# Performance work log

Measured on AMD Instinct MI355X. Metric: run time of the kernel, lower is better.

Reference implementation:

```python
import jax, jax.numpy as jnp
import numpy as np

EPS = 1e-5
QB = 128.0  # 2**(bit-1), bit=8

def _int8_wrap(q):
    # Emulate torch's .to(torch.int8) two's-complement wrap (e.g. 128 -> -128).
    return jnp.mod(q + 128.0, 256.0) - 128.0

def setup_inputs() -> dict:
    key = jax.random.key(0)
    k1, k2, k3 = jax.random.split(key, 3)
    x = jax.random.normal(k1, (4, 2048, 2048), dtype=jnp.float32)
    weights = jax.random.normal(k2, (8192, 2048), dtype=jnp.float32)
    bias = jax.random.normal(k3, (8192,), dtype=jnp.float32)
    return {"x": x, "weights": weights, "bias": bias}

def reference(x, weights, bias):
    in_features = x.shape[-1]
    out_features = weights.shape[0]
    # LayerNorm over last dim, no affine (F.layer_norm defaults, eps=1e-5)
    mu = jnp.mean(x, axis=-1, keepdims=True)
    var = jnp.mean(jnp.square(x - mu), axis=-1, keepdims=True)
    input_norm = (x - mu) * jax.lax.rsqrt(var + EPS)
    # absmax int8 activation quant (nl_next=False path)
    max_val = jnp.max(jnp.abs(input_norm))
    q = _int8_wrap(jnp.round(input_norm * (QB / max_val)))
    dequant = max_val / QB
    # weight sign-binarization around the mean
    weight_quant = jnp.sign(weights - jnp.mean(weights))
    # quantized matmul + dequant scales + bias
    out = jnp.einsum('bsd,od->bso', q, weight_quant)  # [B,S,out]
    beta = jnp.sum(jnp.abs(weights)) / (in_features * out_features)
    out = out * (dequant * beta) + bias
    return out
```

## Files before the change

kernel.cpp:

```cpp
#include <hip/hip_runtime.h>


using i32x4 = __attribute__((ext_vector_type(4))) int;
using i32x16 = __attribute__((ext_vector_type(16))) int;

typedef const __attribute__((address_space(1))) void cg_void;
typedef __attribute__((address_space(3))) void lds_void;

#define K_DIM 2048
#define N_DIM 8192
#define M_DIM 8192
#define NELEM_W 16777216


__global__ __launch_bounds__(256) void pass1(const float* __restrict__ x,
                                             const float4* __restrict__ w4,
                                             float* __restrict__ mu_arr,
                                             float* __restrict__ rstd_arr,
                                             float* __restrict__ rowmax,
                                             double2* __restrict__ part) {
    __shared__ double sbd[8];
    __shared__ float sb1[4];
    __shared__ float sb2[8];
    const int bid = blockIdx.x, t = threadIdx.x;
    const int lane = t & 63, wv = t >> 6;
    if (bid < 1024) {
        double s = 0.0, a = 0.0;
        for (int i = bid * 256 + t; i < NELEM_W / 4; i += 1024 * 256) {
            float4 v = w4[i];
            s += (double)v.x + (double)v.y + (double)v.z + (double)v.w;
            a += fabs((double)v.x) + fabs((double)v.y) + fabs((double)v.z) + fabs((double)v.w);
        }
        for (int o = 32; o; o >>= 1) { s += __shfl_xor(s, o); a += __shfl_xor(a, o); }
        if (lane == 0) { sbd[wv] = s; sbd[4 + wv] = a; }
        __syncthreads();
        if (t == 0) {
            double2 r;
            r.x = sbd[0] + sbd[1] + sbd[2] + sbd[3];
            r.y = sbd[4] + sbd[5] + sbd[6] + sbd[7];
            part[bid] = r;
        }
    } else {
        const int row = bid - 1024;
        const float4* xr = (const float4*)x + (size_t)row * 512;
        float4 v0 = xr[t], v1 = xr[t + 256];
        float s = v0.x + v0.y + v0.z + v0.w + v1.x + v1.y + v1.z + v1.w;
        for (int o = 32; o; o >>= 1) s += __shfl_xor(s, o);
        if (lane == 0) sb1[wv] = s;
        __syncthreads();
        float mu = (sb1[0] + sb1[1] + sb1[2] + sb1[3]) * (1.0f / 2048.0f);
        float ssq = 0.f, md = 0.f, d;
        d = v0.x - mu; ssq += d * d; md = fmaxf(md, fabsf(d));
        d = v0.y - mu; ssq += d * d; md = fmaxf(md, fabsf(d));
        d = v0.z - mu; ssq += d * d; md = fmaxf(md, fabsf(d));
        d = v0.w - mu; ssq += d * d; md = fmaxf(md, fabsf(d));
        d = v1.x - mu; ssq += d * d; md = fmaxf(md, fabsf(d));
        d = v1.y - mu; ssq += d * d; md = fmaxf(md, fabsf(d));
        d = v1.z - mu; ssq += d * d; md = fmaxf(md, fabsf(d));
        d = v1.w - mu; ssq += d * d; md = fmaxf(md, fabsf(d));
        for (int o = 32; o; o >>= 1) {
            ssq += __shfl_xor(ssq, o);
            md = fmaxf(md, __shfl_xor(md, o));
        }
        if (lane == 0) { sb2[wv] = ssq; sb2[4 + wv] = md; }
        __syncthreads();
        if (t == 0) {
            float var = (sb2[0] + sb2[1] + sb2[2] + sb2[3]) * (1.0f / 2048.0f);
            float rstd = 1.0f / sqrtf(var + 1e-5f);
            mu_arr[row] = mu;
            rstd_arr[row] = rstd;
            rowmax[row] = fmaxf(fmaxf(sb2[4], sb2[5]), fmaxf(sb2[6], sb2[7])) * rstd;
        }
    }
}

__global__ __launch_bounds__(256) void wred2(const double2* __restrict__ part,
                                             const float* __restrict__ rowmax,
                                             unsigned* __restrict__ scal) {
    double s = 0.0, a = 0.0;
    float m = 0.f;
    const int t = threadIdx.x, lane = t & 63, wv = t >> 6;
    for (int i = t; i < 1024; i += 256) { double2 p = part[i]; s += p.x; a += p.y; }
    for (int i = t; i < 8192; i += 256) m = fmaxf(m, rowmax[i]);
    for (int o = 32; o; o >>= 1) {
        s += __shfl_xor(s, o); a += __shfl_xor(a, o);
        m = fmaxf(m, __shfl_xor(m, o));
    }
    __shared__ double sbd[8];
    __shared__ float sbm[4];
    if (lane == 0) { sbd[wv] = s; sbd[4 + wv] = a; sbm[wv] = m; }
    __syncthreads();
    if (t == 0) {
        double st = sbd[0] + sbd[1] + sbd[2] + sbd[3];
        double at = sbd[4] + sbd[5] + sbd[6] + sbd[7];
        ((float*)scal)[0] = fmaxf(fmaxf(sbm[0], sbm[1]), fmaxf(sbm[2], sbm[3]));
        ((float*)scal)[1] = (float)(st / (double)NELEM_W);
        ((float*)scal)[2] = (float)(at / (double)NELEM_W);
    }
}

__device__ __forceinline__ int sgn8(float d) { return (d > 0.f) ? 1 : ((d < 0.f) ? -1 : 0); }

__global__ __launch_bounds__(256) void pass2(const float* __restrict__ x,
                                             const float4* __restrict__ w4,
                                             const float* __restrict__ mu_arr,
                                             const float* __restrict__ rstd_arr,
                                             const unsigned* __restrict__ scal,
                                             signed char* __restrict__ q,
                                             int4* __restrict__ wq4) {
    const int bid = blockIdx.x, t = threadIdx.x;
    if (bid < 1024) {
        float wm = ((const float*)scal)[1];
        for (int i = bid * 256 + t; i < NELEM_W / 16; i += 1024 * 256) {
            int words[4];
            #pragma unroll
            for (int jj = 0; jj < 4; ++jj) {
                float4 v = w4[i * 4 + jj];
                int b0 = sgn8(v.x - wm) & 255, b1 = sgn8(v.y - wm) & 255;
                int b2 = sgn8(v.z - wm) & 255, b3 = sgn8(v.w - wm) & 255;
                words[jj] = b0 | (b1 << 8) | (b2 << 16) | (b3 << 24);
            }
            wq4[i] = make_int4(words[0], words[1], words[2], words[3]);
        }
    } else {
        const int row = bid - 1024;
        float mu = mu_arr[row], rstd = rstd_arr[row];
        float s = 128.0f / ((const float*)scal)[0];
        const float4* xr = (const float4*)x + (size_t)row * 512;
        float4 v0 = xr[2 * t], v1 = xr[2 * t + 1];
        float xs[8] = {v0.x, v0.y, v0.z, v0.w, v1.x, v1.y, v1.z, v1.w};
        int b[8];
        #pragma unroll
        for (int j = 0; j < 8; ++j) {
            float norm = (xs[j] - mu) * rstd;
            int qi = (int)rintf(norm * s);
            b[j] = qi & 255;
        }
        int w0 = b[0] | (b[1] << 8) | (b[2] << 16) | (b[3] << 24);
        int w1 = b[4] | (b[5] << 8) | (b[6] << 16) | (b[7] << 24);
        ((int2*)(q + (size_t)row * 2048))[t] = make_int2(w0, w1);
    }
}

#define LD16(p) (*(const i32x4*)(p))
#define TILE_BYTES 24576

#define STAGE(koff, sbase)                                                                  \
    do {                                                                                    \
        __builtin_amdgcn_global_load_lds((cg_void*)(gA + (koff)),                           \
            (lds_void*)(lds + (sbase) + w * 2048), 16, 0, 0);                               \
        __builtin_amdgcn_global_load_lds((cg_void*)(gA + 8 * K_DIM + (koff)),               \
            (lds_void*)(lds + (sbase) + w * 2048 + 1024), 16, 0, 0);                        \
        __builtin_amdgcn_global_load_lds((cg_void*)(gB + (koff)),                           \
            (lds_void*)(lds + (sbase) + 16384 + w * 1024), 16, 0, 0);                       \
    } while (0)

__global__ __launch_bounds__(512, 4) void gemm_i8(const signed char* __restrict__ A,
                                                  const signed char* __restrict__ B,
                                                  const float* __restrict__ bias,
                                                  const unsigned* __restrict__ scal,
                                                  float* __restrict__ C) {
    __shared__ alignas(16) char lds[49152];
    const int t = threadIdx.x, w = t >> 6, lane = t & 63;

    const int wg = blockIdx.x;
    const int xcd = wg & 7, idx = wg >> 3;
    const int bm = (xcd * 4 + (idx >> 6)) * 256;
    const int bn = (idx & 63) * 128;

    const int wr = w >> 1, wc = w & 1;
    const int r32 = lane & 31, hi = lane >> 5;

    const int uu = (lane & 7) ^ (lane >> 3);
    const int aRow = w * 16 + (lane >> 3) + ((uu >> 2) << 7);
    const int bRow = w * 8 + (lane >> 3) + ((uu >> 2) << 6);
    const int gcol = (uu & 3) << 4;
    const signed char* gA = A + (size_t)(bm + aRow) * K_DIM + gcol;
    const signed char* gB = B + (size_t)(bn + bRow) * K_DIM + gcol;

    const char* aBase = lds + ((wr & 1) * 64 + r32) * 128;
    const char* bBase = lds + 16384 + r32 * 128;
    const int axr = r32 & 7;
    const int aS0 = ((((wr >> 1) << 2) + hi) ^ axr) << 4;
    const int aS1 = ((((wr >> 1) << 2) + 2 + hi) ^ axr) << 4;
    const int bS0 = (((wc << 2) + hi) ^ axr) << 4;
    const int bS1 = (((wc << 2) + 2 + hi) ^ axr) << 4;

    const float scale = (((const float*)scal)[0] * (1.0f / 128.0f)) * ((const float*)scal)[2];

    i32x16 acc[2][2] = {};
    i32x4 a0[2], a1[2], b0[2], b1[2];

    STAGE(0, 0);

    #pragma unroll 2
    for (int kt = 0; kt < 32; ++kt) {
        const int c = (kt & 1) * TILE_BYTES;
        if (kt < 31) {
            STAGE((kt + 1) * 64, ((kt + 1) & 1) * TILE_BYTES);
            asm volatile("s_waitcnt vmcnt(3)" ::: "memory");
        } else {
            asm volatile("s_waitcnt vmcnt(0)" ::: "memory");
        }
        __builtin_amdgcn_s_barrier();

        #pragma unroll
        for (int mb = 0; mb < 2; ++mb) a0[mb] = LD16(aBase + c + mb * 4096 + aS0);
        #pragma unroll
        for (int nb = 0; nb < 2; ++nb) b0[nb] = LD16(bBase + c + nb * 4096 + bS0);
        #pragma unroll
        for (int mb = 0; mb < 2; ++mb) a1[mb] = LD16(aBase + c + mb * 4096 + aS1);
        #pragma unroll
        for (int nb = 0; nb < 2; ++nb) b1[nb] = LD16(bBase + c + nb * 4096 + bS1);
        __builtin_amdgcn_s_setprio(1);
        #pragma unroll
        for (int mb = 0; mb < 2; ++mb)
            #pragma unroll
            for (int nb = 0; nb < 2; ++nb)
                acc[mb][nb] = __builtin_amdgcn_mfma_i32_32x32x32_i8(a0[mb], b0[nb],
                                                                    acc[mb][nb], 0, 0, 0);
        #pragma unroll
        for (int mb = 0; mb < 2; ++mb)
            #pragma unroll
            for (int nb = 0; nb < 2; ++nb)
                acc[mb][nb] = __builtin_amdgcn_mfma_i32_32x32x32_i8(a1[mb], b1[nb],
                                                                    acc[mb][nb], 0, 0, 0);
        __builtin_amdgcn_s_setprio(0);
        __builtin_amdgcn_s_barrier();
    }

    const int colbase = bn + wc * 64;
    float bi[2];
    #pragma unroll
    for (int nb = 0; nb < 2; ++nb) bi[nb] = bias[colbase + nb * 32 + r32];
    #pragma unroll
    for (int mb = 0; mb < 2; ++mb) {
        #pragma unroll
        for (int nb = 0; nb < 2; ++nb) {
            #pragma unroll
            for (int r = 0; r < 16; ++r) {
                int row = bm + wr * 64 + mb * 32 + (r & 3) + 8 * (r >> 2) + 4 * hi;
                int col = colbase + nb * 32 + r32;
                C[(size_t)row * N_DIM + col] = (float)acc[mb][nb][r] * scale + bi[nb];
            }
        }
    }
}

extern "C" void kernel_launch(void* const* d_in, const int* in_sizes, int n_in,
                              void* d_out, int out_size, void* d_ws, size_t ws_size,
                              hipStream_t stream) {
    const float* x = (const float*)d_in[0];
    const float* wts = (const float*)d_in[1];
    const float* bias = (const float*)d_in[2];
    float* out = (float*)d_out;

    char* ws = (char*)d_ws;
    unsigned* scal = (unsigned*)ws;
    double2* part = (double2*)(ws + 1024);
    float* mu = (float*)(ws + 32768);
    float* rstd = (float*)(ws + 65536);
    float* rowmax = (float*)(ws + 98304);
    signed char* q = (signed char*)(ws + 131072);
    signed char* wq = (signed char*)(ws + 131072 + 16777216);

    hipLaunchKernelGGL(pass1, dim3(9216), dim3(256), 0, stream,
                       x, (const float4*)wts, mu, rstd, rowmax, part);
    hipLaunchKernelGGL(wred2, dim3(1), dim3(256), 0, stream, part, rowmax, scal);
    hipLaunchKernelGGL(pass2, dim3(9216), dim3(256), 0, stream,
                       x, (const float4*)wts, mu, rstd, scal, q, (int4*)wq);
    hipLaunchKernelGGL(gemm_i8, dim3(2048), dim3(512), 0, stream,
                       q, wq, bias, scal, out);
}
```

Measured before the change: 226.9 us.

## Load B fragments directly from global into registers, stage only A in LDS

The GEMM no longer stages the binarized weight tile B through shared memory. Each wave loads its B fragments straight from global memory into registers every k-step, while A stays double-buffered in LDS under a new XOR swizzle. The LDS footprint drops from 48KB to 32KB and B's LDS write/read traffic is removed. In exchange, duplicate B global loads across waves (wr rows) rely on L1/L2 hits, and the load latency is exposed inside the loop with only loose vmcnt waits.

```diff
diff --git a/kernel.cpp b/kernel.cpp
--- a/kernel.cpp
+++ b/kernel.cpp
@@ -143,7 +143,7 @@
 }
 
 #define LD16(p) (*(const i32x4*)(p))
-#define TILE_BYTES 24576
+#define TILE_BYTES 16384
 
 #define STAGE(koff, sbase)                                                                  \
     do {                                                                                    \
@@ -151,8 +151,6 @@
             (lds_void*)(lds + (sbase) + w * 2048), 16, 0, 0);                               \
         __builtin_amdgcn_global_load_lds((cg_void*)(gA + 8 * K_DIM + (koff)),               \
             (lds_void*)(lds + (sbase) + w * 2048 + 1024), 16, 0, 0);                        \
-        __builtin_amdgcn_global_load_lds((cg_void*)(gB + (koff)),                           \
-            (lds_void*)(lds + (sbase) + 16384 + w * 1024), 16, 0, 0);                       \
     } while (0)
 
 __global__ __launch_bounds__(512, 4) void gemm_i8(const signed char* __restrict__ A,
@@ -160,7 +158,7 @@
                                                   const float* __restrict__ bias,
                                                   const unsigned* __restrict__ scal,
                                                   float* __restrict__ C) {
-    __shared__ alignas(16) char lds[49152];
+    __shared__ alignas(16) char lds[32768];
     const int t = threadIdx.x, w = t >> 6, lane = t & 63;
 
     const int wg = blockIdx.x;
@@ -171,59 +169,70 @@
     const int wr = w >> 1, wc = w & 1;
     const int r32 = lane & 31, hi = lane >> 5;
 
-    const int uu = (lane & 7) ^ (lane >> 3);
-    const int aRow = w * 16 + (lane >> 3) + ((uu >> 2) << 7);
-    const int bRow = w * 8 + (lane >> 3) + ((uu >> 2) << 6);
-    const int gcol = (uu & 3) << 4;
-    const signed char* gA = A + (size_t)(bm + aRow) * K_DIM + gcol;
-    const signed char* gB = B + (size_t)(bn + bRow) * K_DIM + gcol;
+    const int g0 = lane >> 3, s0 = lane & 7;
+    const int u0 = s0 ^ g0 ^ (((w * 2) & 3) << 1);
+    const int u1 = s0 ^ g0 ^ (((w * 2 + 1) & 3) << 1);
+    const int aRow0 = w * 16 + g0 + ((u0 >> 2) << 7);
+    const int aRow1 = w * 16 + 8 + g0 + ((u1 >> 2) << 7);
+    const signed char* gA  = A + (size_t)(bm + aRow0) * K_DIM + ((u0 & 3) << 4);
+    const signed char* gA1 = A + (size_t)(bm + aRow1) * K_DIM + ((u1 & 3) << 4) - 8 * K_DIM;
+    #define gA_J1 gA1
+
+    const signed char* gBf = B + (size_t)(bn + wc * 64 + r32) * K_DIM + hi * 16;
 
     const char* aBase = lds + ((wr & 1) * 64 + r32) * 128;
-    const char* bBase = lds + 16384 + r32 * 128;
-    const int axr = r32 & 7;
-    const int aS0 = ((((wr >> 1) << 2) + hi) ^ axr) << 4;
-    const int aS1 = ((((wr >> 1) << 2) + 2 + hi) ^ axr) << 4;
-    const int bS0 = (((wc << 2) + hi) ^ axr) << 4;
-    const int bS1 = (((wc << 2) + 2 + hi) ^ axr) << 4;
+    const int aperm = (r32 & 7) ^ (((r32 >> 3) & 3) << 1);
+    const int aS0 = ((((wr >> 1) << 2) + hi) ^ aperm) << 4;
+    const int aS1 = ((((wr >> 1) << 2) + 2 + hi) ^ aperm) << 4;
 
     const float scale = (((const float*)scal)[0] * (1.0f / 128.0f)) * ((const float*)scal)[2];
 
     i32x16 acc[2][2] = {};
-    i32x4 a0[2], a1[2], b0[2], b1[2];
-
-    STAGE(0, 0);
+    i32x4 af0[2], af1[2], bc[2][2];
+
+    {
+        __builtin_amdgcn_global_load_lds((cg_void*)(gA), (lds_void*)(lds + w * 2048), 16, 0, 0);
+        __builtin_amdgcn_global_load_lds((cg_void*)(gA1 + 8 * K_DIM),
+                                         (lds_void*)(lds + w * 2048 + 1024), 16, 0, 0);
+    }
 
     #pragma unroll 2
     for (int kt = 0; kt < 32; ++kt) {
         const int c = (kt & 1) * TILE_BYTES;
+        #pragma unroll
+        for (int nb = 0; nb < 2; ++nb)
+            #pragma unroll
+            for (int ks = 0; ks < 2; ++ks)
+                bc[nb][ks] = LD16(gBf + (size_t)nb * 65536 + kt * 64 + ks * 32);
         if (kt < 31) {
-            STAGE((kt + 1) * 64, ((kt + 1) & 1) * TILE_BYTES);
-            asm volatile("s_waitcnt vmcnt(3)" ::: "memory");
+            const int koff = (kt + 1) * 64;
+            const int sb = ((kt + 1) & 1) * TILE_BYTES;
+            __builtin_amdgcn_global_load_lds((cg_void*)(gA + koff),
+                (lds_void*)(lds + sb + w * 2048), 16, 0, 0);
+            __builtin_amdgcn_global_load_lds((cg_void*)(gA1 + 8 * K_DIM + koff),
+                (lds_void*)(lds + sb + w * 2048 + 1024), 16, 0, 0);
+            asm volatile("s_waitcnt vmcnt(6)" ::: "memory");
         } else {
-            asm volatile("s_waitcnt vmcnt(0)" ::: "memory");
+            asm volatile("s_waitcnt vmcnt(4)" ::: "memory");
         }
         __builtin_amdgcn_s_barrier();
 
         #pragma unroll
-        for (int mb = 0; mb < 2; ++mb) a0[mb] = LD16(aBase + c + mb * 4096 + aS0);
-        #pragma unroll
-        for (int nb = 0; nb < 2; ++nb) b0[nb] = LD16(bBase + c + nb * 4096 + bS0);
-        #pragma unroll
-        for (int mb = 0; mb < 2; ++mb) a1[mb] = LD16(aBase + c + mb * 4096 + aS1);
-        #pragma unroll
-        for (int nb = 0; nb < 2; ++nb) b1[nb] = LD16(bBase + c + nb * 4096 + bS1);
+        for (int mb = 0; mb < 2; ++mb) af0[mb] = LD16(aBase + c + mb * 4096 + aS0);
+        #pragma unroll
+        for (int mb = 0; mb < 2; ++mb) af1[mb] = LD16(aBase + c + mb * 4096 + aS1);
         __builtin_amdgcn_s_setprio(1);
         #pragma unroll
         for (int mb = 0; mb < 2; ++mb)
             #pragma unroll
             for (int nb = 0; nb < 2; ++nb)
-                acc[mb][nb] = __builtin_amdgcn_mfma_i32_32x32x32_i8(a0[mb], b0[nb],
+                acc[mb][nb] = __builtin_amdgcn_mfma_i32_32x32x32_i8(af0[mb], bc[nb][0],
                                                                     acc[mb][nb], 0, 0, 0);
         #pragma unroll
         for (int mb = 0; mb < 2; ++mb)
             #pragma unroll
             for (int nb = 0; nb < 2; ++nb)
-                acc[mb][nb] = __builtin_amdgcn_mfma_i32_32x32x32_i8(a1[mb], b1[nb],
+                acc[mb][nb] = __builtin_amdgcn_mfma_i32_32x32x32_i8(af1[mb], bc[nb][1],
                                                                     acc[mb][nb], 0, 0, 0);
         __builtin_amdgcn_s_setprio(0);
         __builtin_amdgcn_s_barrier();
```

Measured after the change: 369.5 us. 62.8% more time.
